# Performance work log

Measured on AMD Instinct MI355X. Metric: run time of the kernel, lower is better.

The kernel has to match this reference:

```python
import jax, jax.numpy as jnp
import numpy as np

B, P, N, E, H, KD, M = 64, 100, 1000, 512, 8, 64, 10
SQRT_E = float(np.sqrt(E))
CLIP = 10.0


def _heads(x):
    # [b, n, H*KD] -> [b, H, n, KD]
    b, n, _ = x.shape
    return x.reshape(b, n, H, KD).transpose(0, 2, 1, 3)


def setup_inputs() -> dict:
    key = jax.random.key(0)
    ks = jax.random.split(key, 20)
    f = jnp.float32
    s = 0.02  # weight init scale
    return {
        "encoded_last_node": jax.random.normal(ks[0], (B, P, E), f),
        "encoded_last_agents": jax.random.normal(ks[1], (B, P, E), f),
        "cur_dist": jax.random.uniform(ks[2], (B, P, N), f, 1e-3, 1.0),
        "ninf_mask": jnp.zeros((B, P, N), f),
        "lengths": jax.random.uniform(ks[3], (B, P, M), f),
        "max_dis": jax.random.uniform(ks[4], (B, P, 1), f),
        "remain_max_dis": jax.random.uniform(ks[5], (B, P, 1), f),
        "q_first": 0.5 * jax.random.normal(ks[6], (B, H, P, KD), f),
        "k": 0.5 * jax.random.normal(ks[7], (B, H, N, KD), f),
        "v": 0.5 * jax.random.normal(ks[8], (B, H, N, KD), f),
        "single_head_key": 0.5 * jax.random.normal(ks[9], (B, E, N), f),
        "Wq_last_w": s * jax.random.normal(ks[10], (H * KD, 2 * E + 2), f),
        "dis_emb_w": s * jax.random.normal(ks[11], (H * KD, 4), f),
        "mh_w": s * jax.random.normal(ks[12], (E, H * KD), f),
        "mh_b": s * jax.random.normal(ks[13], (E,), f),
        "dist_alpha": jnp.ones((1,), f),
        "depot_num": jax.random.randint(ks[14], (B,), 1, M + 1),
        "route_cnt": jax.random.randint(ks[15], (B, P, 1), 0, M),
        "left_city": jax.random.randint(ks[16], (B, P), 0, N + 1),
        "city_num": N,
    }


def reference(encoded_last_node, encoded_last_agents, cur_dist, ninf_mask,
              lengths, max_dis, remain_max_dis, q_first, k, v, single_head_key,
              Wq_last_w, dis_emb_w, mh_w, mh_b, dist_alpha,
              depot_num, route_cnt, left_city, city_num):
    # route_num = depot_num - 1, broadcast to route_cnt shape [B,P,1]
    route_num = jnp.broadcast_to(depot_num[:, None, None], route_cnt.shape) - 1
    g_cur = jnp.take_along_axis(lengths, route_cnt, axis=-1)    # [B,P,1]
    g_route = jnp.take_along_axis(lengths, route_num, axis=-1)  # [B,P,1]
    q_info_in = jnp.concatenate([g_cur, g_route, max_dis, remain_max_dis], axis=-1)  # [B,P,4]
    q_info = _heads(q_info_in @ dis_emb_w.T)  # [B,H,P,KD]

    frac = 1.0 - (route_cnt + 1).astype(jnp.float32) / (route_num + 1).astype(jnp.float32)
    lc = left_city[:, :, None].astype(jnp.float32) / city_num
    q_last_in = jnp.concatenate([encoded_last_node, encoded_last_agents, frac, lc], axis=-1)  # [B,P,2E+2]
    q_last = _heads(q_last_in @ Wq_last_w.T)  # [B,H,P,KD]

    q = q_first + q_last + q_info  # [B,H,P,KD]

    # masked multi-head attention (rank3 ninf mask)
    score = jnp.einsum("bhpd,bhnd->bhpn", q, k) / jnp.sqrt(jnp.float32(KD))
    score = score + ninf_mask[:, None, :, :]
    w = jax.nn.softmax(score, axis=-1)
    out = jnp.einsum("bhpn,bhnd->bhpd", w, v)
    out_concat = out.transpose(0, 2, 1, 3).reshape(out.shape[0], out.shape[2], H * KD)  # [B,P,H*KD]
    mh = out_concat @ mh_w.T + mh_b  # [B,P,E]

    # single-head distance-biased scoring
    score2 = jnp.einsum("bpe,ben->bpn", mh, single_head_key)  # [B,P,N]
    max_dist = jnp.max(cur_dist, axis=-1, keepdims=True)
    cur_dist_out = -cur_dist / max_dist
    score_clipped = CLIP * jnp.tanh(score2 / SQRT_E + dist_alpha * cur_dist_out)
    probs = jax.nn.softmax(score_clipped + ninf_mask, axis=-1)
    return probs
```

## Files before the change

kernel.cpp:

```cpp
#include <hip/hip_runtime.h>
#include <hip/hip_bf16.h>

#define BB 64
#define PP 100
#define NN 1000
#define EE 512
#define HH 8
#define KDD 64
#define MM 10
#define ROWS (BB*PP)
#define K1K 1026
#define INVSQE 0.044194173824159216f
#define CLIPV 10.0f

union F4 { float4 v; float f[4]; };

using bf16x8 = __attribute__((ext_vector_type(8))) short;
using f32x4  = __attribute__((ext_vector_type(4))) float;

__device__ inline unsigned short f2bf(float x) {
  unsigned u = __float_as_uint(x);
  u += 0x7FFFu + ((u >> 16) & 1u);
  return (unsigned short)(u >> 16);
}

__device__ inline float bf2f(unsigned short s) {
  return __uint_as_float(((unsigned)s) << 16);
}

__device__ inline float fast_tanh(float x) {
  float e = __expf(2.0f * x);
  return 1.0f - 2.0f / (e + 1.0f);
}

__global__ __launch_bounds__(256) void k_rowmax(const float* __restrict__ cd,
                                                float* __restrict__ rmax) {
  int row = blockIdx.x * 4 + (threadIdx.x >> 6);
  int lane = threadIdx.x & 63;
  const float* src = cd + (size_t)row * NN;
  float m = -1e30f;
  for (int i = lane; i < NN; i += 64) m = fmaxf(m, src[i]);
  #pragma unroll
  for (int off = 32; off; off >>= 1) m = fmaxf(m, __shfl_xor(m, off));
  if (lane == 0) rmax[row] = m;
}

__global__ __launch_bounds__(256) void k_qgemm(
    const float* __restrict__ eln, const float* __restrict__ ela,
    const float* __restrict__ lengths, const float* __restrict__ max_dis,
    const float* __restrict__ remain, const float* __restrict__ q_first,
    const float* __restrict__ Wq, const float* __restrict__ dis_emb,
    const int* __restrict__ depot, const int* __restrict__ route_cnt,
    const int* __restrict__ left_city, const int* __restrict__ city_num,
    float* __restrict__ qout) {
  __shared__ unsigned short Xs[64][72];
  __shared__ unsigned short Ws[64][72];
  __shared__ float info_s[64][4];
  __shared__ float fl_s[64][2];
  const int t = threadIdx.x;
  const int lane = t & 63;
  const int w = t >> 6;
  const int lr = lane & 15, lg = lane >> 4;
  const int rowBase = blockIdx.y * 64, colBase = blockIdx.x * 64;

  if (t < 64) {
    int row = rowBase + t;
    int b = row / PP;
    int rc = route_cnt[row];
    int rn = depot[b] - 1;
    info_s[t][0] = lengths[row * MM + rc];
    info_s[t][1] = lengths[row * MM + rn];
    info_s[t][2] = max_dis[row];
    info_s[t][3] = remain[row];
    fl_s[t][0] = 1.0f - (float)(rc + 1) / (float)(rn + 1);
    fl_s[t][1] = (float)left_city[row] / (float)city_num[0];
  }

  f32x4 acc[4];
  #pragma unroll
  for (int m = 0; m < 4; ++m) { acc[m][0] = 0.f; acc[m][1] = 0.f; acc[m][2] = 0.f; acc[m][3] = 0.f; }

  for (int kt = 0; kt < 16; ++kt) {
    const float* xsrc = (kt < 8) ? eln : ela;
    const int koff = (kt & 7) * 64;
    __syncthreads();
    #pragma unroll
    for (int i = 0; i < 4; ++i) {
      int s = i * 256 + t;
      int r = s >> 4, c4 = (s & 15) * 4;
      F4 xv, wv;
      xv.v = *(const float4*)&xsrc[(size_t)(rowBase + r) * 512 + koff + c4];
      wv.v = *(const float4*)&Wq[(size_t)(colBase + r) * K1K + kt * 64 + c4];
      unsigned short* xd = &Xs[r][c4];
      unsigned short* wd = &Ws[r][c4];
      xd[0] = f2bf(xv.f[0]); xd[1] = f2bf(xv.f[1]); xd[2] = f2bf(xv.f[2]); xd[3] = f2bf(xv.f[3]);
      wd[0] = f2bf(wv.f[0]); wd[1] = f2bf(wv.f[1]); wd[2] = f2bf(wv.f[2]); wd[3] = f2bf(wv.f[3]);
    }
    __syncthreads();
    #pragma unroll
    for (int kb = 0; kb < 2; ++kb) {
      bf16x8 bfr = *(bf16x8*)&Ws[w * 16 + lr][kb * 32 + lg * 8];
      #pragma unroll
      for (int m = 0; m < 4; ++m) {
        bf16x8 af = *(bf16x8*)&Xs[m * 16 + lr][kb * 32 + lg * 8];
        acc[m] = __builtin_amdgcn_mfma_f32_16x16x32_bf16(af, bfr, acc[m], 0, 0, 0);
      }
    }
  }

  const int o = colBase + w * 16 + lr;
  F4 de; de.v = *(const float4*)&dis_emb[(size_t)o * 4];
  const float wq1024 = Wq[(size_t)o * K1K + 1024];
  const float wq1025 = Wq[(size_t)o * K1K + 1025];
  const int h = o >> 6, kd = o & 63;
  #pragma unroll
  for (int m = 0; m < 4; ++m) {
    #pragma unroll
    for (int j = 0; j < 4; ++j) {
      int r = m * 16 + lg * 4 + j;
      int row = rowBase + r;
      int b = row / PP, p = row % PP;
      F4 inf; inf.v = *(const float4*)&info_s[r][0];
      float v = acc[m][j]
              + inf.f[0] * de.f[0] + inf.f[1] * de.f[1]
              + inf.f[2] * de.f[2] + inf.f[3] * de.f[3]
              + fl_s[r][0] * wq1024 + fl_s[r][1] * wq1025
              + q_first[(((size_t)b * HH + h) * PP + p) * KDD + kd];
      qout[(size_t)row * 512 + o] = v;
    }
  }
}

__global__ __launch_bounds__(256) void k_attn(
    const float* __restrict__ qin, const float* __restrict__ kk,
    const float* __restrict__ vv, const float* __restrict__ mask,
    float* __restrict__ attn_out) {
  __shared__ unsigned short Kl[64][72];
  __shared__ unsigned short Vt[64][72];
  __shared__ unsigned short PMb[64][72];

  const int t = threadIdx.x;
  const int lane = t & 63;
  const int w = t >> 6;
  const int lr = lane & 15, lg = lane >> 4;
  const int gid = blockIdx.x;
  const int b = gid & 63;
  const int X = gid >> 6;
  const int h = X & 7, half = X >> 3;
  const int bh = b * HH + h;
  const int p0 = half * 64;
  const int nrows = (half == 0) ? 64 : (PP - 64);
  const bool active = (w * 16 < nrows);

  #pragma unroll
  for (int i = 0; i < 4; ++i) {
    int idx = i * 256 + t;
    int r = idx >> 4, c4 = (idx & 15) * 4;
    int p = p0 + r;
    F4 qv; qv.v = make_float4(0.f, 0.f, 0.f, 0.f);
    if (p < PP) qv.v = *(const float4*)&qin[((size_t)(b * PP + p)) * 512 + h * 64 + c4];
    unsigned short* d = &PMb[r][c4];
    d[0] = f2bf(qv.f[0] * 0.125f); d[1] = f2bf(qv.f[1] * 0.125f);
    d[2] = f2bf(qv.f[2] * 0.125f); d[3] = f2bf(qv.f[3] * 0.125f);
  }
  __syncthreads();

  bf16x8 qf[2];
  qf[0] = *(bf16x8*)&PMb[w * 16 + lr][lg * 8];
  qf[1] = *(bf16x8*)&PMb[w * 16 + lr][32 + lg * 8];
  __syncthreads();

  float Lacc[4] = {0.f, 0.f, 0.f, 0.f};
  f32x4 Oa[4];
  #pragma unroll
  for (int dt = 0; dt < 4; ++dt) { Oa[dt][0] = 0.f; Oa[dt][1] = 0.f; Oa[dt][2] = 0.f; Oa[dt][3] = 0.f; }

  for (int ch = 0; ch < 16; ++ch) {
    const int n0 = ch * 64;

    #pragma unroll
    for (int i = 0; i < 4; ++i) {
      int idx = i * 256 + t;
      int r = idx >> 4, c4 = (idx & 15) * 4;
      int n = n0 + r;
      F4 kv; kv.v = make_float4(0.f, 0.f, 0.f, 0.f);
      if (n < NN) kv.v = *(const float4*)&kk[(((size_t)bh * NN) + n) * 64 + c4];
      unsigned short* d = &Kl[r][c4];
      d[0] = f2bf(kv.f[0]); d[1] = f2bf(kv.f[1]); d[2] = f2bf(kv.f[2]); d[3] = f2bf(kv.f[3]);
    }
    {
      int b2 = t & 15, a = t >> 4;
      F4 rowv[4];
      #pragma unroll
      for (int r = 0; r < 4; ++r) {
        int n = n0 + 4 * b2 + r;
        rowv[r].v = (n < NN) ? *(const float4*)&vv[(((size_t)bh * NN) + n) * 64 + 4 * a]
                             : make_float4(0.f, 0.f, 0.f, 0.f);
      }
      #pragma unroll
      for (int c = 0; c < 4; ++c) {
        unsigned short* dst = &Vt[4 * a + c][4 * b2];
        dst[0] = f2bf(rowv[0].f[c]); dst[1] = f2bf(rowv[1].f[c]);
        dst[2] = f2bf(rowv[2].f[c]); dst[3] = f2bf(rowv[3].f[c]);
      }
    }
    #pragma unroll
    for (int i = 0; i < 4; ++i) {
      int idx = i * 256 + t;
      int r = idx >> 4, c4 = (idx & 15) * 4;
      if (r < nrows) {
        int p = p0 + r, n = n0 + c4;
        F4 mv;
        if (n + 3 < NN) {
          mv.v = *(const float4*)&mask[((size_t)(b * PP + p)) * NN + n];
        } else {
          #pragma unroll
          for (int j = 0; j < 4; ++j)
            mv.f[j] = (n + j < NN) ? mask[((size_t)(b * PP + p)) * NN + n + j] : -1e30f;
        }
        unsigned short* d = &PMb[r][c4];
        d[0] = f2bf(mv.f[0]); d[1] = f2bf(mv.f[1]); d[2] = f2bf(mv.f[2]); d[3] = f2bf(mv.f[3]);
      }
    }
    __syncthreads();

    if (active) {
      f32x4 sa[4];
      #pragma unroll
      for (int nb = 0; nb < 4; ++nb) { sa[nb][0] = 0.f; sa[nb][1] = 0.f; sa[nb][2] = 0.f; sa[nb][3] = 0.f; }
      #pragma unroll
      for (int kb = 0; kb < 2; ++kb)
        #pragma unroll
        for (int nb = 0; nb < 4; ++nb) {
          bf16x8 kf = *(bf16x8*)&Kl[nb * 16 + lr][kb * 32 + lg * 8];
          sa[nb] = __builtin_amdgcn_mfma_f32_16x16x32_bf16(qf[kb], kf, sa[nb], 0, 0, 0);
        }
      #pragma unroll
      for (int j = 0; j < 4; ++j) {
        int pr = w * 16 + lg * 4 + j;
        #pragma unroll
        for (int nb = 0; nb < 4; ++nb) {
          float mv = bf2f(PMb[pr][nb * 16 + lr]);
          float e = __expf(sa[nb][j] + mv);
          Lacc[j] += e;
          PMb[pr][nb * 16 + lr] = f2bf(e);
        }
      }
      #pragma unroll
      for (int kb = 0; kb < 2; ++kb) {
        bf16x8 pf = *(bf16x8*)&PMb[w * 16 + lr][kb * 32 + lg * 8];
        #pragma unroll
        for (int dt = 0; dt < 4; ++dt) {
          bf16x8 vf = *(bf16x8*)&Vt[dt * 16 + lr][kb * 32 + lg * 8];
          Oa[dt] = __builtin_amdgcn_mfma_f32_16x16x32_bf16(pf, vf, Oa[dt], 0, 0, 0);
        }
      }
    }
    __syncthreads();
  }

  if (active) {
    #pragma unroll
    for (int j = 0; j < 4; ++j) {
      float L = Lacc[j];
      #pragma unroll
      for (int off = 1; off < 16; off <<= 1) L += __shfl_xor(L, off);
      int p = p0 + w * 16 + lg * 4 + j;
      if (p < PP) {
        float inv = (L > 0.f) ? 1.0f / L : 0.f;
        #pragma unroll
        for (int dt = 0; dt < 4; ++dt)
          attn_out[((size_t)(b * PP + p)) * 512 + h * 64 + dt * 16 + lr] = Oa[dt][j] * inv;
      }
    }
  }
}

__global__ __launch_bounds__(256) void k_mhgemm(
    const float* __restrict__ A, const float* __restrict__ W,
    const float* __restrict__ bias, float* __restrict__ out) {
  __shared__ unsigned short Xs[64][72];
  __shared__ unsigned short Ws[64][72];
  const int t = threadIdx.x;
  const int lane = t & 63;
  const int w = t >> 6;
  const int lr = lane & 15, lg = lane >> 4;
  const int rowBase = blockIdx.y * 64, colBase = blockIdx.x * 64;

  f32x4 acc[4];
  #pragma unroll
  for (int m = 0; m < 4; ++m) { acc[m][0] = 0.f; acc[m][1] = 0.f; acc[m][2] = 0.f; acc[m][3] = 0.f; }

  for (int kt = 0; kt < 8; ++kt) {
    const int koff = kt * 64;
    __syncthreads();
    #pragma unroll
    for (int i = 0; i < 4; ++i) {
      int s = i * 256 + t;
      int r = s >> 4, c4 = (s & 15) * 4;
      F4 xv, wv;
      xv.v = *(const float4*)&A[(size_t)(rowBase + r) * 512 + koff + c4];
      wv.v = *(const float4*)&W[(size_t)(colBase + r) * 512 + koff + c4];
      unsigned short* xd = &Xs[r][c4];
      unsigned short* wd = &Ws[r][c4];
      xd[0] = f2bf(xv.f[0]); xd[1] = f2bf(xv.f[1]); xd[2] = f2bf(xv.f[2]); xd[3] = f2bf(xv.f[3]);
      wd[0] = f2bf(wv.f[0]); wd[1] = f2bf(wv.f[1]); wd[2] = f2bf(wv.f[2]); wd[3] = f2bf(wv.f[3]);
    }
    __syncthreads();
    #pragma unroll
    for (int kb = 0; kb < 2; ++kb) {
      bf16x8 bfr = *(bf16x8*)&Ws[w * 16 + lr][kb * 32 + lg * 8];
      #pragma unroll
      for (int m = 0; m < 4; ++m) {
        bf16x8 af = *(bf16x8*)&Xs[m * 16 + lr][kb * 32 + lg * 8];
        acc[m] = __builtin_amdgcn_mfma_f32_16x16x32_bf16(af, bfr, acc[m], 0, 0, 0);
      }
    }
  }

  const int o = colBase + w * 16 + lr;
  const float bv = bias[o];
  #pragma unroll
  for (int m = 0; m < 4; ++m) {
    #pragma unroll
    for (int j = 0; j < 4; ++j) {
      int row = rowBase + m * 16 + lg * 4 + j;
      out[(size_t)row * 512 + o] = acc[m][j] + bv;
    }
  }
}

__global__ __launch_bounds__(256) void k_final_score(
    const float* __restrict__ mh, const float* __restrict__ shk,
    const float* __restrict__ cur_dist, const float* __restrict__ rmax,
    const float* __restrict__ mask, const float* __restrict__ dist_alpha,
    float* __restrict__ sc_out) {
  __shared__ unsigned short As[112][72];
  __shared__ unsigned short Bt[64][72];
  const int t = threadIdx.x;
  const int lane = t & 63;
  const int w = t >> 6;
  const int lr = lane & 15, lg = lane >> 4;
  const int n0 = blockIdx.x * 64, b = blockIdx.y;

  f32x4 acc[7];
  #pragma unroll
  for (int m = 0; m < 7; ++m) { acc[m][0] = 0.f; acc[m][1] = 0.f; acc[m][2] = 0.f; acc[m][3] = 0.f; }

  for (int kt = 0; kt < 8; ++kt) {
    const int k0 = kt * 64;
    __syncthreads();
    #pragma unroll
    for (int i = 0; i < 7; ++i) {
      int s = i * 256 + t;
      if (s < 1792) {
        int r = s >> 4, c4 = (s & 15) * 4;
        F4 xv; xv.v = make_float4(0.f, 0.f, 0.f, 0.f);
        if (r < PP) xv.v = *(const float4*)&mh[(size_t)(b * PP + r) * 512 + k0 + c4];
        unsigned short* xd = &As[r][c4];
        xd[0] = f2bf(xv.f[0]); xd[1] = f2bf(xv.f[1]); xd[2] = f2bf(xv.f[2]); xd[3] = f2bf(xv.f[3]);
      }
    }
    {
      int a = t & 15, kb = t >> 4;
      F4 rowv[4];
      #pragma unroll
      for (int r = 0; r < 4; ++r) {
        int k = k0 + 4 * kb + r;
        int n = n0 + 4 * a;
        rowv[r].v = (n < NN) ? *(const float4*)&shk[((size_t)b * EE + k) * NN + n]
                             : make_float4(0.f, 0.f, 0.f, 0.f);
      }
      #pragma unroll
      for (int c = 0; c < 4; ++c) {
        unsigned short* dst = &Bt[4 * a + c][4 * kb];
        dst[0] = f2bf(rowv[0].f[c]); dst[1] = f2bf(rowv[1].f[c]);
        dst[2] = f2bf(rowv[2].f[c]); dst[3] = f2bf(rowv[3].f[c]);
      }
    }
    __syncthreads();
    #pragma unroll
    for (int kb = 0; kb < 2; ++kb) {
      bf16x8 bfr = *(bf16x8*)&Bt[w * 16 + lr][kb * 32 + lg * 8];
      #pragma unroll
      for (int m = 0; m < 7; ++m) {
        bf16x8 af = *(bf16x8*)&As[m * 16 + lr][kb * 32 + lg * 8];
        acc[m] = __builtin_amdgcn_mfma_f32_16x16x32_bf16(af, bfr, acc[m], 0, 0, 0);
      }
    }
  }

  const float alpha = dist_alpha[0];
  const int n = n0 + w * 16 + lr;
  if (n < NN) {
    #pragma unroll
    for (int m = 0; m < 7; ++m) {
      #pragma unroll
      for (int j = 0; j < 4; ++j) {
        int p = m * 16 + lg * 4 + j;
        if (p >= PP) continue;
        size_t rb = (size_t)(b * PP + p) * NN;
        float rmx = rmax[b * PP + p];
        float cd = cur_dist[rb + n];
        float mk = mask[rb + n];
        sc_out[rb + n] = CLIPV * fast_tanh(acc[m][j] * INVSQE - alpha * cd / rmx) + mk;
      }
    }
  }
}

__global__ __launch_bounds__(256) void k_softmax(const float* __restrict__ sc,
                                                 float* __restrict__ out) {
  __shared__ float redsum[4];
  const int row = blockIdx.x;
  const int t = threadIdx.x;
  const float* src = sc + (size_t)row * NN;
  float e[4];
  float s = 0.f;
  #pragma unroll
  for (int i = 0; i < 4; ++i) {
    int n = i * 256 + t;
    e[i] = (n < NN) ? __expf(src[n]) : 0.f;
    s += e[i];
  }
  #pragma unroll
  for (int off = 32; off; off >>= 1) s += __shfl_xor(s, off);
  int wid = t >> 6, lane = t & 63;
  if (lane == 0) redsum[wid] = s;
  __syncthreads();
  s = redsum[0] + redsum[1] + redsum[2] + redsum[3];
  float inv = 1.0f / s;
  #pragma unroll
  for (int i = 0; i < 4; ++i) {
    int n = i * 256 + t;
    if (n < NN) out[(size_t)row * NN + n] = e[i] * inv;
  }
}

extern "C" void kernel_launch(void* const* d_in, const int* in_sizes, int n_in,
                              void* d_out, int out_size, void* d_ws, size_t ws_size,
                              hipStream_t stream) {
  const float* eln       = (const float*)d_in[0];
  const float* ela       = (const float*)d_in[1];
  const float* cur_dist  = (const float*)d_in[2];
  const float* ninf      = (const float*)d_in[3];
  const float* lengths   = (const float*)d_in[4];
  const float* max_dis   = (const float*)d_in[5];
  const float* remain    = (const float*)d_in[6];
  const float* q_first   = (const float*)d_in[7];
  const float* kten      = (const float*)d_in[8];
  const float* vten      = (const float*)d_in[9];
  const float* shk       = (const float*)d_in[10];
  const float* Wq        = (const float*)d_in[11];
  const float* dis_emb   = (const float*)d_in[12];
  const float* mh_w      = (const float*)d_in[13];
  const float* mh_b      = (const float*)d_in[14];
  const float* dalpha    = (const float*)d_in[15];
  const int*   depot     = (const int*)d_in[16];
  const int*   route_cnt = (const int*)d_in[17];
  const int*   left_city = (const int*)d_in[18];
  const int*   city_num  = (const int*)d_in[19];
  float* out = (float*)d_out;

  float* ws      = (float*)d_ws;
  float* q_ws    = ws;
  float* attn_ws = q_ws + (size_t)ROWS * 512;
  float* mh_ws   = attn_ws + (size_t)ROWS * 512;
  float* sc_ws   = mh_ws + (size_t)ROWS * 512;
  float* rmax_ws = sc_ws + (size_t)ROWS * NN;

  k_rowmax<<<ROWS / 4, 256, 0, stream>>>(cur_dist, rmax_ws);
  k_qgemm<<<dim3(8, 100), 256, 0, stream>>>(eln, ela, lengths, max_dis, remain,
                                            q_first, Wq, dis_emb, depot, route_cnt,
                                            left_city, city_num, q_ws);
  k_attn<<<1024, 256, 0, stream>>>(q_ws, kten, vten, ninf, attn_ws);
  k_mhgemm<<<dim3(8, 100), 256, 0, stream>>>(attn_ws, mh_w, mh_b, mh_ws);
  k_final_score<<<dim3(16, 64), 256, 0, stream>>>(mh_ws, shk, cur_dist, rmax_ws,
                                                  ninf, dalpha, sc_ws);
  k_softmax<<<ROWS, 256, 0, stream>>>(sc_ws, out);
}
```

Baseline: 279.6 us.

## Store intermediate q, attention output and mh activations as bf16

The intermediate buffers passed between kernels (q, attention output, mh projection) are now written in bf16 rather than fp32, and the consumers load them with 8-wide bf16 vector loads straight into shared memory instead of converting fp32 floats. This halves the global traffic for these intermediates and removes the per-element conversions in the consumer loaders. The 1/sqrt(KD) scale moves from the q load into the exp argument via an fma. Precision drops slightly because q and the final-score input are rounded to bf16 once earlier, though the consumers already converted these values to bf16 for the MFMA.

```diff
diff --git a/kernel.cpp b/kernel.cpp
--- a/kernel.cpp
+++ b/kernel.cpp
@@ -33,6 +33,13 @@
   return 1.0f - 2.0f / (e + 1.0f);
 }
 
+__device__ inline bf16x8 bf8_zero() {
+  bf16x8 v;
+  #pragma unroll
+  for (int i = 0; i < 8; ++i) v[i] = 0;
+  return v;
+}
+
 __global__ __launch_bounds__(256) void k_rowmax(const float* __restrict__ cd,
                                                 float* __restrict__ rmax) {
   int row = blockIdx.x * 4 + (threadIdx.x >> 6);
@@ -52,7 +59,7 @@
     const float* __restrict__ Wq, const float* __restrict__ dis_emb,
     const int* __restrict__ depot, const int* __restrict__ route_cnt,
     const int* __restrict__ left_city, const int* __restrict__ city_num,
-    float* __restrict__ qout) {
+    unsigned short* __restrict__ qout) {
   __shared__ unsigned short Xs[64][72];
   __shared__ unsigned short Ws[64][72];
   __shared__ float info_s[64][4];
@@ -126,15 +133,15 @@
               + inf.f[2] * de.f[2] + inf.f[3] * de.f[3]
               + fl_s[r][0] * wq1024 + fl_s[r][1] * wq1025
               + q_first[(((size_t)b * HH + h) * PP + p) * KDD + kd];
-      qout[(size_t)row * 512 + o] = v;
+      qout[(size_t)row * 512 + o] = f2bf(v);
     }
   }
 }
 
 __global__ __launch_bounds__(256) void k_attn(
-    const float* __restrict__ qin, const float* __restrict__ kk,
+    const unsigned short* __restrict__ qin, const float* __restrict__ kk,
     const float* __restrict__ vv, const float* __restrict__ mask,
-    float* __restrict__ attn_out) {
+    unsigned short* __restrict__ attn_out) {
   __shared__ unsigned short Kl[64][72];
   __shared__ unsigned short Vt[64][72];
   __shared__ unsigned short PMb[64][72];
@@ -153,15 +160,13 @@
   const bool active = (w * 16 < nrows);
 
   #pragma unroll
-  for (int i = 0; i < 4; ++i) {
+  for (int i = 0; i < 2; ++i) {
     int idx = i * 256 + t;
-    int r = idx >> 4, c4 = (idx & 15) * 4;
+    int r = idx >> 3, c8 = (idx & 7) * 8;
     int p = p0 + r;
-    F4 qv; qv.v = make_float4(0.f, 0.f, 0.f, 0.f);
-    if (p < PP) qv.v = *(const float4*)&qin[((size_t)(b * PP + p)) * 512 + h * 64 + c4];
-    unsigned short* d = &PMb[r][c4];
-    d[0] = f2bf(qv.f[0] * 0.125f); d[1] = f2bf(qv.f[1] * 0.125f);
-    d[2] = f2bf(qv.f[2] * 0.125f); d[3] = f2bf(qv.f[3] * 0.125f);
+    bf16x8 qv = bf8_zero();
+    if (p < PP) qv = *(const bf16x8*)&qin[((size_t)(b * PP + p)) * 512 + h * 64 + c8];
+    *(bf16x8*)&PMb[r][c8] = qv;
   }
   __syncthreads();
 
@@ -241,7 +246,7 @@
         #pragma unroll
         for (int nb = 0; nb < 4; ++nb) {
           float mv = bf2f(PMb[pr][nb * 16 + lr]);
-          float e = __expf(sa[nb][j] + mv);
+          float e = __expf(fmaf(sa[nb][j], 0.125f, mv));
           Lacc[j] += e;
           PMb[pr][nb * 16 + lr] = f2bf(e);
         }
@@ -270,15 +275,15 @@
         float inv = (L > 0.f) ? 1.0f / L : 0.f;
         #pragma unroll
         for (int dt = 0; dt < 4; ++dt)
-          attn_out[((size_t)(b * PP + p)) * 512 + h * 64 + dt * 16 + lr] = Oa[dt][j] * inv;
+          attn_out[((size_t)(b * PP + p)) * 512 + h * 64 + dt * 16 + lr] = f2bf(Oa[dt][j] * inv);
       }
     }
   }
 }
 
 __global__ __launch_bounds__(256) void k_mhgemm(
-    const float* __restrict__ A, const float* __restrict__ W,
-    const float* __restrict__ bias, float* __restrict__ out) {
+    const unsigned short* __restrict__ A, const float* __restrict__ W,
+    const float* __restrict__ bias, unsigned short* __restrict__ out) {
   __shared__ unsigned short Xs[64][72];
   __shared__ unsigned short Ws[64][72];
   const int t = threadIdx.x;
@@ -295,15 +300,19 @@
     const int koff = kt * 64;
     __syncthreads();
     #pragma unroll
+    for (int i = 0; i < 2; ++i) {
+      int idx = i * 256 + t;
+      int r = idx >> 3, c8 = (idx & 7) * 8;
+      *(bf16x8*)&Xs[r][c8] =
+          *(const bf16x8*)&A[(size_t)(rowBase + r) * 512 + koff + c8];
+    }
+    #pragma unroll
     for (int i = 0; i < 4; ++i) {
       int s = i * 256 + t;
       int r = s >> 4, c4 = (s & 15) * 4;
-      F4 xv, wv;
-      xv.v = *(const float4*)&A[(size_t)(rowBase + r) * 512 + koff + c4];
+      F4 wv;
       wv.v = *(const float4*)&W[(size_t)(colBase + r) * 512 + koff + c4];
-      unsigned short* xd = &Xs[r][c4];
       unsigned short* wd = &Ws[r][c4];
-      xd[0] = f2bf(xv.f[0]); xd[1] = f2bf(xv.f[1]); xd[2] = f2bf(xv.f[2]); xd[3] = f2bf(xv.f[3]);
       wd[0] = f2bf(wv.f[0]); wd[1] = f2bf(wv.f[1]); wd[2] = f2bf(wv.f[2]); wd[3] = f2bf(wv.f[3]);
     }
     __syncthreads();
@@ -325,13 +334,13 @@
     #pragma unroll
     for (int j = 0; j < 4; ++j) {
       int row = rowBase + m * 16 + lg * 4 + j;
-      out[(size_t)row * 512 + o] = acc[m][j] + bv;
+      out[(size_t)row * 512 + o] = f2bf(acc[m][j] + bv);
     }
   }
 }
 
 __global__ __launch_bounds__(256) void k_final_score(
-    const float* __restrict__ mh, const float* __restrict__ shk,
+    const unsigned short* __restrict__ mh, const float* __restrict__ shk,
     const float* __restrict__ cur_dist, const float* __restrict__ rmax,
     const float* __restrict__ mask, const float* __restrict__ dist_alpha,
     float* __restrict__ sc_out) {
@@ -351,14 +360,13 @@
     const int k0 = kt * 64;
     __syncthreads();
     #pragma unroll
-    for (int i = 0; i < 7; ++i) {
-      int s = i * 256 + t;
-      if (s < 1792) {
-        int r = s >> 4, c4 = (s & 15) * 4;
-        F4 xv; xv.v = make_float4(0.f, 0.f, 0.f, 0.f);
-        if (r < PP) xv.v = *(const float4*)&mh[(size_t)(b * PP + r) * 512 + k0 + c4];
-        unsigned short* xd = &As[r][c4];
-        xd[0] = f2bf(xv.f[0]); xd[1] = f2bf(xv.f[1]); xd[2] = f2bf(xv.f[2]); xd[3] = f2bf(xv.f[3]);
+    for (int i = 0; i < 4; ++i) {
+      int idx = i * 256 + t;
+      if (idx < 896) {
+        int r = idx >> 3, c8 = (idx & 7) * 8;
+        bf16x8 v = bf8_zero();
+        if (r < PP) v = *(const bf16x8*)&mh[(size_t)(b * PP + r) * 512 + k0 + c8];
+        *(bf16x8*)&As[r][c8] = v;
       }
     }
     {
@@ -462,11 +470,11 @@
   const int*   city_num  = (const int*)d_in[19];
   float* out = (float*)d_out;
 
-  float* ws      = (float*)d_ws;
-  float* q_ws    = ws;
-  float* attn_ws = q_ws + (size_t)ROWS * 512;
-  float* mh_ws   = attn_ws + (size_t)ROWS * 512;
-  float* sc_ws   = mh_ws + (size_t)ROWS * 512;
+  float* ws = (float*)d_ws;
+  unsigned short* q_ws    = (unsigned short*)ws;
+  unsigned short* attn_ws = (unsigned short*)(ws + (size_t)ROWS * 512);
+  unsigned short* mh_ws   = (unsigned short*)(ws + (size_t)2 * ROWS * 512);
+  float* sc_ws   = ws + (size_t)3 * ROWS * 512;
   float* rmax_ws = sc_ws + (size_t)ROWS * NN;
 
   k_rowmax<<<ROWS / 4, 256, 0, stream>>>(cur_dist, rmax_ws);
```

Result: faster. 264.1 us (-5.5%).
